# Kernel optimization log

Measured on AMD Instinct MI355X. Metric: run time of the kernel, lower is better.

## Reference

```python
import jax, jax.numpy as jnp
import numpy as np

N_NODES = 100000
N_EDGES = 1600000
IN_DIM = 128
HEADS = 4
OUT_DIM = 32
NEG_SLOPE = 0.2


def setup_inputs() -> dict:
    key = jax.random.key(0)
    k1, k2, k3, k4, k5, k6 = jax.random.split(key, 6)
    x = jax.random.normal(k1, (N_NODES, IN_DIM), dtype=jnp.float32)
    src = jax.random.randint(k2, (N_EDGES,), 0, N_NODES)
    dst = jax.random.randint(k3, (N_EDGES,), 0, N_NODES)
    edge_index = jnp.stack([src, dst]).astype(jnp.int64)
    # xavier-ish scaled params
    W = jax.random.normal(k4, (HEADS * OUT_DIM, IN_DIM), dtype=jnp.float32) * (2.0 / (IN_DIM + HEADS * OUT_DIM)) ** 0.5
    att_src = jax.random.normal(k5, (HEADS, OUT_DIM), dtype=jnp.float32) * (2.0 / (HEADS + OUT_DIM)) ** 0.5
    att_dst = jax.random.normal(k6, (HEADS, OUT_DIM), dtype=jnp.float32) * (2.0 / (HEADS + OUT_DIM)) ** 0.5
    bias = jnp.zeros((HEADS * OUT_DIM,), dtype=jnp.float32)
    return {"x": x, "edge_index": edge_index, "W": W, "att_src": att_src, "att_dst": att_dst, "bias": bias}


def reference(x, edge_index, W, att_src, att_dst, bias):
    n_nodes = x.shape[0]
    src, dst = edge_index[0], edge_index[1]
    # linear projection: [N, H, D]
    x_proj = (x @ W.T).reshape(n_nodes, HEADS, OUT_DIM)
    # per-edge attention logits: [E, H]
    att = (x_proj[src] * att_src).sum(-1) + (x_proj[dst] * att_dst).sum(-1)
    att = jnp.where(att >= 0, att, NEG_SLOPE * att)  # leaky_relu
    # segment softmax over incoming edges per destination node
    max_per_node = jax.ops.segment_max(att, dst, num_segments=n_nodes)
    max_per_node = jnp.maximum(max_per_node, -1e15)  # match torch init for empty segments
    exp_scores = jnp.exp(att - max_per_node[dst])
    denom = jax.ops.segment_sum(exp_scores, dst, num_segments=n_nodes)
    alpha = exp_scores / (denom[dst] + 1e-12)  # [E, H]
    # weighted scatter-add aggregation
    messages = x_proj[src] * alpha[:, :, None]  # [E, H, D]
    out = jax.ops.segment_sum(messages.reshape(-1, HEADS * OUT_DIM), dst, num_segments=n_nodes)
    return out + bias
```

## Files before the change

kernel.cpp:

```cpp
#include <hip/hip_runtime.h>
#include <math.h>

#define N_NODES 100000
#define N_EDGES 1600000
#define IN_DIM 128
#define HEADS 4
#define OUT_DIM 32
#define HD 128
#define NEG_SLOPE 0.2f

#define EBLK 2048
#define NBLK_E 782
#define NBIN 391
#define GH_TOT (NBIN * NBLK_E)
#define S1_BLKS 150

typedef __attribute__((ext_vector_type(8))) short short8;
typedef __attribute__((ext_vector_type(4))) float f32x4;

__device__ inline ushort f2bf(float f) {
    uint u = __float_as_uint(f);
    u += 0x7fffu + ((u >> 16) & 1u);
    return (ushort)(u >> 16);
}

__global__ __launch_bounds__(256) void k_gemm(const float* __restrict__ x,
                                              const float* __restrict__ W,
                                              ushort* __restrict__ xp,
                                              const float* __restrict__ att_src,
                                              const float* __restrict__ att_dst,
                                              float* __restrict__ asrc,
                                              float* __restrict__ adst) {
    __shared__ ushort lA[64 * 128];
    __shared__ ushort lB[128 * 128];
    const int tid = threadIdx.x;
    const long row_base = (long)blockIdx.x * 64;

    {
        const int r = tid >> 2;
        const int c0 = (tid & 3) * 32;
        const long row = row_base + r;
        const float* src = x + row * IN_DIM + c0;
#pragma unroll
        for (int i = 0; i < 4; i++) {
            float4 va, vb;
            if (row < N_NODES) {
                va = *(const float4*)(src + 8 * i);
                vb = *(const float4*)(src + 8 * i + 4);
            } else {
                va = make_float4(0.f, 0.f, 0.f, 0.f);
                vb = va;
            }
            ushort h[8] = {f2bf(va.x), f2bf(va.y), f2bf(va.z), f2bf(va.w),
                           f2bf(vb.x), f2bf(vb.y), f2bf(vb.z), f2bf(vb.w)};
            uint byte = (uint)(r * 256 + (c0 + 8 * i) * 2);
            byte ^= (uint)((r & 7) << 4);
            *(uint4*)((char*)lA + byte) = *(const uint4*)h;
        }
    }
    {
        const int c = tid >> 1;
        const int k0 = (tid & 1) * 64;
        const float* src = W + c * IN_DIM + k0;
#pragma unroll
        for (int i = 0; i < 8; i++) {
            float4 va = *(const float4*)(src + 8 * i);
            float4 vb = *(const float4*)(src + 8 * i + 4);
            ushort h[8] = {f2bf(va.x), f2bf(va.y), f2bf(va.z), f2bf(va.w),
                           f2bf(vb.x), f2bf(vb.y), f2bf(vb.z), f2bf(vb.w)};
            uint byte = (uint)(c * 256 + (k0 + 8 * i) * 2);
            byte ^= (uint)((c & 7) << 4);
            *(uint4*)((char*)lB + byte) = *(const uint4*)h;
        }
    }
    __syncthreads();

    const int w = tid >> 6;
    const int lane = tid & 63;
    const int l15 = lane & 15;
    const int g8 = (lane >> 4) * 8;
    const int arow = w * 16 + l15;

    f32x4 acc[8];
#pragma unroll
    for (int nt = 0; nt < 8; nt++) acc[nt] = (f32x4){0.f, 0.f, 0.f, 0.f};

#pragma unroll
    for (int t = 0; t < 4; t++) {
        uint ab = (uint)(arow * 256 + (t * 32 + g8) * 2);
        ab ^= (uint)((arow & 7) << 4);
        short8 af = *(const short8*)((const char*)lA + ab);
#pragma unroll
        for (int nt = 0; nt < 8; nt++) {
            int c = nt * 16 + l15;
            uint bb = (uint)(c * 256 + (t * 32 + g8) * 2);
            bb ^= (uint)((c & 7) << 4);
            short8 bfr = *(const short8*)((const char*)lB + bb);
            acc[nt] = __builtin_amdgcn_mfma_f32_16x16x32_bf16(af, bfr, acc[nt], 0, 0, 0);
        }
    }
    __syncthreads();

    {
        const int m4 = 4 * (lane >> 4);
#pragma unroll
        for (int nt = 0; nt < 8; nt++) {
            int c = nt * 16 + l15;
#pragma unroll
            for (int r = 0; r < 4; r++) {
                lA[(w * 16 + m4 + r) * 128 + c] = f2bf(acc[nt][r]);
            }
        }
    }
    __syncthreads();

    {
        const int r = tid >> 2;
        const long node = row_base + r;
        if (node < N_NODES) {
            const int h = tid & 3;
            const int c0 = h * 32;
            const uint4* s = (const uint4*)(lA + r * 128 + c0);
            uint4 v0 = s[0], v1 = s[1], v2 = s[2], v3 = s[3];
            uint4* d = (uint4*)(xp + node * HD + c0);
            d[0] = v0; d[1] = v1; d[2] = v2; d[3] = v3;
            const float* as = att_src + c0;
            const float* ad = att_dst + c0;
            float s0 = 0.f, s1 = 0.f;
            uint4 vv[4] = {v0, v1, v2, v3};
#pragma unroll
            for (int q = 0; q < 4; q++) {
                const uint* u = (const uint*)&vv[q];
#pragma unroll
                for (int p = 0; p < 4; p++) {
                    float f0 = __uint_as_float((u[p] & 0xffffu) << 16);
                    float f1 = __uint_as_float(u[p] & 0xffff0000u);
                    int cc = q * 8 + p * 2;
                    s0 = fmaf(f0, as[cc], s0);
                    s0 = fmaf(f1, as[cc + 1], s0);
                    s1 = fmaf(f0, ad[cc], s1);
                    s1 = fmaf(f1, ad[cc + 1], s1);
                }
            }
            asrc[node * HEADS + h] = s0;
            adst[node * HEADS + h] = s1;
        }
    }
}

__global__ __launch_bounds__(256) void k_chist(const int* __restrict__ ei,
                                               int* __restrict__ ghist) {
    __shared__ int h[NBIN];
    const int tid = threadIdx.x;
    for (int i = tid; i < NBIN; i += 256) h[i] = 0;
    __syncthreads();
    const int base = blockIdx.x * EBLK;
#pragma unroll
    for (int i = 0; i < 8; i++) {
        int e = base + tid + i * 256;
        if (e < N_EDGES) atomicAdd(&h[ei[N_EDGES + e] >> 8], 1);
    }
    __syncthreads();
    for (int i = tid; i < NBIN; i += 256) ghist[i * NBLK_E + blockIdx.x] = h[i];
}

__global__ __launch_bounds__(256) void k_s1(int* __restrict__ g, int* __restrict__ part) {
    __shared__ int lds[256];
    const int tid = threadIdx.x;
    const int base = blockIdx.x * 2048 + tid * 8;
    int v[8];
    int s = 0;
#pragma unroll
    for (int i = 0; i < 8; i++) {
        v[i] = (base + i < GH_TOT) ? g[base + i] : 0;
        s += v[i];
    }
    lds[tid] = s;
    __syncthreads();
    for (int o = 1; o < 256; o <<= 1) {
        int u = (tid >= o) ? lds[tid - o] : 0;
        __syncthreads();
        lds[tid] += u;
        __syncthreads();
    }
    int run = (tid == 0) ? 0 : lds[tid - 1];
#pragma unroll
    for (int i = 0; i < 8; i++) {
        int t = v[i];
        if (base + i < GH_TOT) g[base + i] = run;
        run += t;
    }
    if (tid == 255) part[blockIdx.x] = lds[255];
}

__global__ __launch_bounds__(256) void k_s2(int* __restrict__ part) {
    __shared__ int lds[256];
    const int tid = threadIdx.x;
    int v = (tid < S1_BLKS) ? part[tid] : 0;
    lds[tid] = v;
    __syncthreads();
    for (int o = 1; o < 256; o <<= 1) {
        int u = (tid >= o) ? lds[tid - o] : 0;
        __syncthreads();
        lds[tid] += u;
        __syncthreads();
    }
    if (tid < S1_BLKS) part[tid] = (tid == 0) ? 0 : lds[tid - 1];
}

__global__ __launch_bounds__(256) void k_s3(int* __restrict__ g, const int* __restrict__ part) {
    const int p = part[blockIdx.x];
    const int base = blockIdx.x * 2048;
#pragma unroll
    for (int i = 0; i < 8; i++) {
        int idx = base + threadIdx.x + i * 256;
        if (idx < GH_TOT) g[idx] += p;
    }
}

__global__ __launch_bounds__(256) void k_cscatter(const int* __restrict__ ei,
                                                  const int* __restrict__ ghist,
                                                  int* __restrict__ bpack) {
    __shared__ int base[NBIN];
    const int tid = threadIdx.x;
    for (int i = tid; i < NBIN; i += 256) base[i] = ghist[i * NBLK_E + blockIdx.x];
    __syncthreads();
    const int eb = blockIdx.x * EBLK;
#pragma unroll
    for (int i = 0; i < 8; i++) {
        int e = eb + tid + i * 256;
        if (e < N_EDGES) {
            int d = ei[N_EDGES + e];
            int s = ei[e];
            int p = atomicAdd(&base[d >> 8], 1);
            bpack[p] = (s << 8) | (d & 255);
        }
    }
}

__global__ __launch_bounds__(256) void k_fine(const int* __restrict__ ghist,
                                              const int* __restrict__ bpack,
                                              int* __restrict__ esrc,
                                              int* __restrict__ row_start) {
    __shared__ int cnt[256];
    __shared__ int scn[256];
    __shared__ int off[256];
    const int tid = threadIdx.x;
    const int b = blockIdx.x;
    const int S = ghist[b * NBLK_E];
    const int E = (b == NBIN - 1) ? N_EDGES : ghist[(b + 1) * NBLK_E];
    const int m = E - S;
    cnt[tid] = 0;
    __syncthreads();
    for (int i = tid; i < m; i += 256) atomicAdd(&cnt[bpack[S + i] & 255], 1);
    __syncthreads();
    scn[tid] = cnt[tid];
    __syncthreads();
    for (int o = 1; o < 256; o <<= 1) {
        int u = (tid >= o) ? scn[tid - o] : 0;
        __syncthreads();
        scn[tid] += u;
        __syncthreads();
    }
    const int excl = (tid == 0) ? 0 : scn[tid - 1];
    off[tid] = excl;
    const int node = b * 256 + tid;
    if (node <= N_NODES) row_start[node] = S + excl;
    __syncthreads();
    for (int i = tid; i < m; i += 256) {
        int pk = bpack[S + i];
        int p = atomicAdd(&off[pk & 255], 1);
        esrc[S + p] = pk & ~255;
    }
}

__global__ __launch_bounds__(256) void k_aggregate(const int* __restrict__ row_start,
                                                   const int* __restrict__ esrc,
                                                   const char* __restrict__ asrcB,
                                                   const float4* __restrict__ adst4,
                                                   const char* __restrict__ xpB,
                                                   const float* __restrict__ bias,
                                                   float* __restrict__ out) {
    __shared__ float lw[4][64][4];
    __shared__ int loff[4][64];
    const int wid = threadIdx.x >> 6;
    const int lane = threadIdx.x & 63;
    const int n = blockIdx.x * 4 + wid;
    if (n >= N_NODES) return;
    const int s0 = row_start[n];
    const int s1 = row_start[n + 1];
    const int h = lane >> 4;
    const uint lane4 = (uint)lane * 4;
    const float4 ad = adst4[n];

    float acc0 = 0.f, acc1 = 0.f, den = 0.f;

    for (int base = s0; base < s1; base += 64) {
        const int rem = s1 - base;
        const int cnt = rem < 64 ? rem : 64;
        const bool v = lane < cnt;
        int moff = v ? esrc[base + lane] : 0;
        float4 as = *(const float4*)(asrcB + (moff >> 4));
        float tx = as.x + ad.x, ty = as.y + ad.y, tz = as.z + ad.z, tw = as.w + ad.w;
        tx = (tx >= 0.f) ? tx : NEG_SLOPE * tx;
        ty = (ty >= 0.f) ? ty : NEG_SLOPE * ty;
        tz = (tz >= 0.f) ? tz : NEG_SLOPE * tz;
        tw = (tw >= 0.f) ? tw : NEG_SLOPE * tw;
        float4 wv;
        wv.x = v ? __expf(fminf(tx, 80.f)) : 0.f;
        wv.y = v ? __expf(fminf(ty, 80.f)) : 0.f;
        wv.z = v ? __expf(fminf(tz, 80.f)) : 0.f;
        wv.w = v ? __expf(fminf(tw, 80.f)) : 0.f;
        loff[wid][lane] = moff;
        *(float4*)&lw[wid][lane][0] = wv;

        const int cnt8v = (cnt + 7) & ~7;
        for (int j = 0; j < cnt8v; j += 8) {
            float e0 = lw[wid][j + 0][h], e1 = lw[wid][j + 1][h];
            float e2 = lw[wid][j + 2][h], e3 = lw[wid][j + 3][h];
            float e4 = lw[wid][j + 4][h], e5 = lw[wid][j + 5][h];
            float e6 = lw[wid][j + 6][h], e7 = lw[wid][j + 7][h];
            int4 sv0 = *(const int4*)&loff[wid][j];
            int4 sv1 = *(const int4*)&loff[wid][j + 4];
            uint g0 = *(const uint*)(xpB + ((uint)sv0.x + lane4));
            uint g1 = *(const uint*)(xpB + ((uint)sv0.y + lane4));
            uint g2 = *(const uint*)(xpB + ((uint)sv0.z + lane4));
            uint g3 = *(const uint*)(xpB + ((uint)sv0.w + lane4));
            uint g4 = *(const uint*)(xpB + ((uint)sv1.x + lane4));
            uint g5 = *(const uint*)(xpB + ((uint)sv1.y + lane4));
            uint g6 = *(const uint*)(xpB + ((uint)sv1.z + lane4));
            uint g7 = *(const uint*)(xpB + ((uint)sv1.w + lane4));
            den += ((e0 + e1) + (e2 + e3)) + ((e4 + e5) + (e6 + e7));
            acc0 = fmaf(e0, __uint_as_float(g0 << 16), acc0);
            acc1 = fmaf(e0, __uint_as_float(g0 & 0xffff0000u), acc1);
            acc0 = fmaf(e1, __uint_as_float(g1 << 16), acc0);
            acc1 = fmaf(e1, __uint_as_float(g1 & 0xffff0000u), acc1);
            acc0 = fmaf(e2, __uint_as_float(g2 << 16), acc0);
            acc1 = fmaf(e2, __uint_as_float(g2 & 0xffff0000u), acc1);
            acc0 = fmaf(e3, __uint_as_float(g3 << 16), acc0);
            acc1 = fmaf(e3, __uint_as_float(g3 & 0xffff0000u), acc1);
            acc0 = fmaf(e4, __uint_as_float(g4 << 16), acc0);
            acc1 = fmaf(e4, __uint_as_float(g4 & 0xffff0000u), acc1);
            acc0 = fmaf(e5, __uint_as_float(g5 << 16), acc0);
            acc1 = fmaf(e5, __uint_as_float(g5 & 0xffff0000u), acc1);
            acc0 = fmaf(e6, __uint_as_float(g6 << 16), acc0);
            acc1 = fmaf(e6, __uint_as_float(g6 & 0xffff0000u), acc1);
            acc0 = fmaf(e7, __uint_as_float(g7 << 16), acc0);
            acc1 = fmaf(e7, __uint_as_float(g7 & 0xffff0000u), acc1);
        }
    }
    float inv = 1.f / (den + 1e-12f);
    float2 b2 = ((const float2*)bias)[lane];
    float2 o;
    o.x = acc0 * inv + b2.x;
    o.y = acc1 * inv + b2.y;
    ((float2*)(out + (long)n * HD))[lane] = o;
}

extern "C" void kernel_launch(void* const* d_in, const int* in_sizes, int n_in,
                              void* d_out, int out_size, void* d_ws, size_t ws_size,
                              hipStream_t stream) {
    const float* x = (const float*)d_in[0];
    const int* ei = (const int*)d_in[1];
    const float* W = (const float*)d_in[2];
    const float* att_src = (const float*)d_in[3];
    const float* att_dst = (const float*)d_in[4];
    const float* bias = (const float*)d_in[5];
    float* out = (float*)d_out;
    char* ws = (char*)d_ws;

    ushort* xp       = (ushort*)(ws + 0);
    float* asrc      = (float*)(ws + 25600000);
    float* adst      = (float*)(ws + 27200000);
    int* esrc        = (int*)(ws + 28800000);
    int* bpack       = (int*)(ws + 35200000);
    int* ghist       = (int*)(ws + 41600000);
    int* part        = (int*)(ws + 42823648);
    int* row_start   = (int*)(ws + 42824256);

    k_gemm<<<(N_NODES + 63) / 64, 256, 0, stream>>>(x, W, xp, att_src, att_dst, asrc, adst);
    k_chist<<<NBLK_E, 256, 0, stream>>>(ei, ghist);
    k_s1<<<S1_BLKS, 256, 0, stream>>>(ghist, part);
    k_s2<<<1, 256, 0, stream>>>(part);
    k_s3<<<S1_BLKS, 256, 0, stream>>>(ghist, part);
    k_cscatter<<<NBLK_E, 256, 0, stream>>>(ei, ghist, bpack);
    k_fine<<<NBIN, 256, 0, stream>>>(ghist, bpack, esrc, row_start);
    k_aggregate<<<(N_NODES + 3) / 4, 256, 0, stream>>>(row_start, esrc,
                                                       (const char*)asrc, (const float4*)adst,
                                                       (const char*)xp, bias, out);
}
```

Baseline: 168.5 us.

## Pre-convert W to bf16, load GEMM operands directly, merge scan kernels

W is converted to bf16 once inside the histogram kernel. The GEMM then reads its A fragments straight from global x and its B fragments from the bf16 W buffer, so the LDS staging of A and B and one barrier are gone, and LDS shrinks to a padded output tile. The two-level scan kernels k_s2 and k_s3 are merged: each block reduces the preceding partial sums itself, which removes one launch. The GEMM is moved after the scatter kernel. The trade-off is uncoalesced, redundant global reads of W fragments by every block, which should mostly hit in cache.

Result: slower. 174.2 us (+3.3%).

```diff
diff --git a/kernel.cpp b/kernel.cpp
--- a/kernel.cpp
+++ b/kernel.cpp
@@ -25,61 +25,24 @@
 }
 
 __global__ __launch_bounds__(256) void k_gemm(const float* __restrict__ x,
-                                              const float* __restrict__ W,
+                                              const ushort* __restrict__ wb,
                                               ushort* __restrict__ xp,
                                               const float* __restrict__ att_src,
                                               const float* __restrict__ att_dst,
                                               float* __restrict__ asrc,
                                               float* __restrict__ adst) {
-    __shared__ ushort lA[64 * 128];
-    __shared__ ushort lB[128 * 128];
+    __shared__ ushort lO[64 * 136];
     const int tid = threadIdx.x;
     const long row_base = (long)blockIdx.x * 64;
-
-    {
-        const int r = tid >> 2;
-        const int c0 = (tid & 3) * 32;
-        const long row = row_base + r;
-        const float* src = x + row * IN_DIM + c0;
-#pragma unroll
-        for (int i = 0; i < 4; i++) {
-            float4 va, vb;
-            if (row < N_NODES) {
-                va = *(const float4*)(src + 8 * i);
-                vb = *(const float4*)(src + 8 * i + 4);
-            } else {
-                va = make_float4(0.f, 0.f, 0.f, 0.f);
-                vb = va;
-            }
-            ushort h[8] = {f2bf(va.x), f2bf(va.y), f2bf(va.z), f2bf(va.w),
-                           f2bf(vb.x), f2bf(vb.y), f2bf(vb.z), f2bf(vb.w)};
-            uint byte = (uint)(r * 256 + (c0 + 8 * i) * 2);
-            byte ^= (uint)((r & 7) << 4);
-            *(uint4*)((char*)lA + byte) = *(const uint4*)h;
-        }
-    }
-    {
-        const int c = tid >> 1;
-        const int k0 = (tid & 1) * 64;
-        const float* src = W + c * IN_DIM + k0;
-#pragma unroll
-        for (int i = 0; i < 8; i++) {
-            float4 va = *(const float4*)(src + 8 * i);
-            float4 vb = *(const float4*)(src + 8 * i + 4);
-            ushort h[8] = {f2bf(va.x), f2bf(va.y), f2bf(va.z), f2bf(va.w),
-                           f2bf(vb.x), f2bf(vb.y), f2bf(vb.z), f2bf(vb.w)};
-            uint byte = (uint)(c * 256 + (k0 + 8 * i) * 2);
-            byte ^= (uint)((c & 7) << 4);
-            *(uint4*)((char*)lB + byte) = *(const uint4*)h;
-        }
-    }
-    __syncthreads();
-
     const int w = tid >> 6;
     const int lane = tid & 63;
     const int l15 = lane & 15;
     const int g8 = (lane >> 4) * 8;
     const int arow = w * 16 + l15;
+    const long grow = row_base + arow;
+    const bool rv = grow < N_NODES;
+    const float* xr = x + grow * IN_DIM;
+    const short8* wv = (const short8*)wb;
 
     f32x4 acc[8];
 #pragma unroll
@@ -87,28 +50,29 @@
 
 #pragma unroll
     for (int t = 0; t < 4; t++) {
-        uint ab = (uint)(arow * 256 + (t * 32 + g8) * 2);
-        ab ^= (uint)((arow & 7) << 4);
-        short8 af = *(const short8*)((const char*)lA + ab);
+        float4 a0 = make_float4(0.f, 0.f, 0.f, 0.f), a1 = a0;
+        if (rv) {
+            a0 = *(const float4*)(xr + t * 32 + g8);
+            a1 = *(const float4*)(xr + t * 32 + g8 + 4);
+        }
+        ushort ah[8] = {f2bf(a0.x), f2bf(a0.y), f2bf(a0.z), f2bf(a0.w),
+                        f2bf(a1.x), f2bf(a1.y), f2bf(a1.z), f2bf(a1.w)};
+        short8 af = *(const short8*)ah;
+#pragma unroll
+        for (int nt = 0; nt < 8; nt++) {
+            short8 bfr = wv[(nt * 16 + l15) * 16 + t * 4 + (g8 >> 3)];
+            acc[nt] = __builtin_amdgcn_mfma_f32_16x16x32_bf16(af, bfr, acc[nt], 0, 0, 0);
+        }
+    }
+
+    {
+        const int m4 = 4 * (lane >> 4);
 #pragma unroll
         for (int nt = 0; nt < 8; nt++) {
             int c = nt * 16 + l15;
-            uint bb = (uint)(c * 256 + (t * 32 + g8) * 2);
-            bb ^= (uint)((c & 7) << 4);
-            short8 bfr = *(const short8*)((const char*)lB + bb);
-            acc[nt] = __builtin_amdgcn_mfma_f32_16x16x32_bf16(af, bfr, acc[nt], 0, 0, 0);
-        }
-    }
-    __syncthreads();
-
-    {
-        const int m4 = 4 * (lane >> 4);
-#pragma unroll
-        for (int nt = 0; nt < 8; nt++) {
-            int c = nt * 16 + l15;
 #pragma unroll
             for (int r = 0; r < 4; r++) {
-                lA[(w * 16 + m4 + r) * 128 + c] = f2bf(acc[nt][r]);
+                lO[(w * 16 + m4 + r) * 136 + c] = f2bf(acc[nt][r]);
             }
         }
     }
@@ -120,7 +84,7 @@
         if (node < N_NODES) {
             const int h = tid & 3;
             const int c0 = h * 32;
-            const uint4* s = (const uint4*)(lA + r * 128 + c0);
+            const uint4* s = (const uint4*)(lO + r * 136 + c0);
             uint4 v0 = s[0], v1 = s[1], v2 = s[2], v3 = s[3];
             uint4* d = (uint4*)(xp + node * HD + c0);
             d[0] = v0; d[1] = v1; d[2] = v2; d[3] = v3;
@@ -149,9 +113,17 @@
 }
 
 __global__ __launch_bounds__(256) void k_chist(const int* __restrict__ ei,
-                                               int* __restrict__ ghist) {
+                                               int* __restrict__ ghist,
+                                               const float* __restrict__ W,
+                                               ushort* __restrict__ wb) {
     __shared__ int h[NBIN];
     const int tid = threadIdx.x;
+    if (blockIdx.x < 16) {
+        int i = (blockIdx.x * 256 + tid) * 4;
+        float4 v = *(const float4*)(W + i);
+        ushort o[4] = {f2bf(v.x), f2bf(v.y), f2bf(v.z), f2bf(v.w)};
+        *(ulong1*)(wb + i) = *(const ulong1*)o;
+    }
     for (int i = tid; i < NBIN; i += 256) h[i] = 0;
     __syncthreads();
     const int base = blockIdx.x * EBLK;
@@ -193,27 +165,20 @@
     if (tid == 255) part[blockIdx.x] = lds[255];
 }
 
-__global__ __launch_bounds__(256) void k_s2(int* __restrict__ part) {
-    __shared__ int lds[256];
-    const int tid = threadIdx.x;
-    int v = (tid < S1_BLKS) ? part[tid] : 0;
-    lds[tid] = v;
-    __syncthreads();
-    for (int o = 1; o < 256; o <<= 1) {
-        int u = (tid >= o) ? lds[tid - o] : 0;
-        __syncthreads();
-        lds[tid] += u;
-        __syncthreads();
-    }
-    if (tid < S1_BLKS) part[tid] = (tid == 0) ? 0 : lds[tid - 1];
-}
-
-__global__ __launch_bounds__(256) void k_s3(int* __restrict__ g, const int* __restrict__ part) {
-    const int p = part[blockIdx.x];
+__global__ __launch_bounds__(256) void k_s23(int* __restrict__ g, const int* __restrict__ part) {
+    __shared__ int red[256];
+    const int tid = threadIdx.x;
+    red[tid] = (tid < (int)blockIdx.x && tid < S1_BLKS) ? part[tid] : 0;
+    __syncthreads();
+    for (int o = 128; o > 0; o >>= 1) {
+        if (tid < o) red[tid] += red[tid + o];
+        __syncthreads();
+    }
+    const int p = red[0];
     const int base = blockIdx.x * 2048;
 #pragma unroll
     for (int i = 0; i < 8; i++) {
-        int idx = base + threadIdx.x + i * 256;
+        int idx = base + tid + i * 256;
         if (idx < GH_TOT) g[idx] += p;
     }
 }
@@ -377,13 +342,13 @@
     int* ghist       = (int*)(ws + 41600000);
     int* part        = (int*)(ws + 42823648);
     int* row_start   = (int*)(ws + 42824256);
-
-    k_gemm<<<(N_NODES + 63) / 64, 256, 0, stream>>>(x, W, xp, att_src, att_dst, asrc, adst);
-    k_chist<<<NBLK_E, 256, 0, stream>>>(ei, ghist);
+    ushort* wb       = (ushort*)(ws + 43224272);
+
+    k_chist<<<NBLK_E, 256, 0, stream>>>(ei, ghist, W, wb);
     k_s1<<<S1_BLKS, 256, 0, stream>>>(ghist, part);
-    k_s2<<<1, 256, 0, stream>>>(part);
-    k_s3<<<S1_BLKS, 256, 0, stream>>>(ghist, part);
+    k_s23<<<S1_BLKS, 256, 0, stream>>>(ghist, part);
     k_cscatter<<<NBLK_E, 256, 0, stream>>>(ei, ghist, bpack);
+    k_gemm<<<(N_NODES + 63) / 64, 256, 0, stream>>>(x, wb, xp, att_src, att_dst, asrc, adst);
     k_fine<<<NBIN, 256, 0, stream>>>(ghist, bpack, esrc, row_start);
     k_aggregate<<<(N_NODES + 3) / 4, 256, 0, stream>>>(row_start, esrc,
                                                        (const char*)asrc, (const float4*)adst,
```
